# Kernel optimization log

Measured on AMD Instinct MI355X. Metric: run time of the kernel, lower is better.

The kernel has to match this reference:

```python
import jax, jax.numpy as jnp
import numpy as np

N, IPI, OPI, OPO = 20000, 128, 64, 16

def setup_inputs() -> dict:
    key = jax.random.key(0)
    k1, k2, k3, k4 = jax.random.split(key, 4)
    admat = jax.random.uniform(k1, (N, N), dtype=jnp.float32)
    features = jax.random.normal(k2, (N, IPI), dtype=jnp.float32)
    W1 = jax.random.normal(k3, (IPI, OPI), dtype=jnp.float32) * (1.0 / np.sqrt(IPI))
    W2 = jax.random.normal(k4, (OPI, OPO), dtype=jnp.float32) * (1.0 / np.sqrt(OPI))
    return {"admat": admat, "features": features, "W1": W1, "W2": W2}

def reference(admat, features, W1, W2):
    # layer1: A @ (X @ W1), thin-first ordering to minimize FLOPs/traffic
    h = jax.nn.relu(admat @ (features @ W1))          # [N, OPI]
    logits = admat @ (h @ W2)                          # [N, OPO]
    return jax.nn.softmax(logits, axis=1)
```

## Files before the change

kernel.cpp:

```cpp
#include <hip/hip_runtime.h>
#include <hip/hip_bf16.h>

#define NROWS 20000
#define IPI 128
#define OPI 64
#define OPO 16
#define BK 256
#define BK2 1024
#define A4S 10240

typedef __attribute__((ext_vector_type(8))) short bf16x8;
typedef __attribute__((ext_vector_type(4))) float f32x4;
typedef __attribute__((ext_vector_type(2))) unsigned int u32x2;
typedef __attribute__((ext_vector_type(4))) unsigned int u32x4;

#define LUT_LO 0x3C383000u
#define LUT_HI 0x4C484440u

static __device__ __forceinline__ unsigned short f2bf(float f) {
    __hip_bfloat16 h = __float2bfloat16(f);
    return *reinterpret_cast<unsigned short*>(&h);
}
static __device__ __forceinline__ unsigned pk2(float a, float b) {
    return (unsigned)f2bf(a) | ((unsigned)f2bf(b) << 16);
}
static __device__ __forceinline__ unsigned pk4_fp8(float a, float b, float c, float d) {
    int v = __builtin_amdgcn_cvt_pk_fp8_f32(a, b, 0, false);
    v = __builtin_amdgcn_cvt_pk_fp8_f32(c, d, v, true);
    return (unsigned)v;
}
static __device__ __forceinline__ unsigned char f2fp8(float a) {
    return (unsigned char)(pk4_fp8(a, 0.f, 0.f, 0.f) & 0xff);
}
static __device__ __forceinline__ unsigned nib4(float a) {
    const float q = a * 4.f;
    const float n = (q < 2.5f) ? fminf(rintf(q + q), 4.f)
                               : fminf(rintf(q), 4.f) + 2.f;
    return (unsigned)n;
}
static __device__ __forceinline__ u32x2 exp8(unsigned w) {
    const unsigned sl = w & 0x07070707u;
    const unsigned sh = (w >> 4) & 0x07070707u;
    const unsigned fe = __builtin_amdgcn_perm(LUT_HI, LUT_LO, sl);
    const unsigned fo = __builtin_amdgcn_perm(LUT_HI, LUT_LO, sh);
    u32x2 o;
    o[0] = __builtin_amdgcn_perm(fo, fe, 0x05010400u);
    o[1] = __builtin_amdgcn_perm(fo, fe, 0x07030602u);
    return o;
}

__global__ __launch_bounds__(256)
void k_xw1(const float* __restrict__ X, const float* __restrict__ W1,
           unsigned short* __restrict__ Bt) {
    __shared__ float w1[IPI * OPI];
    const int t = threadIdx.x;
    for (int i = t * 4; i < IPI * OPI; i += 1024)
        *(float4*)&w1[i] = *(const float4*)&W1[i];
    __syncthreads();

    const int r  = blockIdx.x * 16 + (t >> 4);
    const int c4 = (t & 15) * 4;
    const float* xr = X + (size_t)r * IPI;
    float4 acc = make_float4(0.f, 0.f, 0.f, 0.f);
    #pragma unroll 8
    for (int k = 0; k < IPI; ++k) {
        const float x = xr[k];
        const float4 w = *(const float4*)&w1[k * OPI + c4];
        acc.x = fmaf(x, w.x, acc.x);
        acc.y = fmaf(x, w.y, acc.y);
        acc.z = fmaf(x, w.z, acc.z);
        acc.w = fmaf(x, w.w, acc.w);
    }
    Bt[(size_t)(c4 + 0) * NROWS + r] = f2bf(acc.x);
    Bt[(size_t)(c4 + 1) * NROWS + r] = f2bf(acc.y);
    Bt[(size_t)(c4 + 2) * NROWS + r] = f2bf(acc.z);
    Bt[(size_t)(c4 + 3) * NROWS + r] = f2bf(acc.w);
}

__global__ __launch_bounds__(256)
void k_gemm1(const float* __restrict__ A, const unsigned short* __restrict__ Bt,
             float* __restrict__ Out, unsigned char* __restrict__ A4, int KC) {
    __shared__ unsigned short As[64 * BK];
    __shared__ unsigned short Bs[64 * BK];
    const int t    = threadIdx.x;
    const int lane = t & 63;
    const int wid  = t >> 6;
    const int lrow = lane & 15;
    const int lk   = lane >> 4;
    const int brow    = blockIdx.x * 64;
    const int k_begin = blockIdx.y * KC;
    const int k_end   = min(NROWS, k_begin + KC);

    const int sc_c = lane >> 1;
    const int sc_h = (lane & 1) * 4;

    f32x4 acc[4];
    #pragma unroll
    for (int n = 0; n < 4; ++n) acc[n] = (f32x4){0.f, 0.f, 0.f, 0.f};

    f32x4 va[16], vna[16];
    u32x2 vb[16], vnb[16];

    {
        const int  kg  = k_begin + lane * 4;
        const bool kok = kg < k_end;
        #pragma unroll
        for (int i = 0; i < 16; ++i) {
            const int grow = brow + wid * 16 + i;
            va[i] = (f32x4){0.f, 0.f, 0.f, 0.f};
            if (kok && grow < NROWS)
                va[i] = __builtin_nontemporal_load(
                    (const f32x4*)(A + (size_t)grow * NROWS + kg));
            vb[i] = (u32x2){0u, 0u};
            if (kok)
                vb[i] = *(const u32x2*)(Bt + (size_t)(wid * 16 + i) * NROWS + kg);
        }
    }

    for (int kt = k_begin; kt < k_end; kt += BK) {
        #pragma unroll
        for (int i = 0; i < 16; ++i) {
            const int r = wid * 16 + i;
            u32x2 u;
            u[0] = pk2(va[i][0], va[i][1]);
            u[1] = pk2(va[i][2], va[i][3]);
            const int slot = (sc_c ^ (r & 7)) * 8 + sc_h;
            *(u32x2*)&As[r * BK + slot] = u;
            *(u32x2*)&Bs[r * BK + slot] = vb[i];
        }
        __syncthreads();

        {
            const int  kgn  = kt + BK + lane * 4;
            const bool nok  = kgn < k_end;
            #pragma unroll
            for (int i = 0; i < 16; ++i) {
                const int grow = brow + wid * 16 + i;
                vna[i] = (f32x4){0.f, 0.f, 0.f, 0.f};
                if (nok && grow < NROWS)
                    vna[i] = __builtin_nontemporal_load(
                        (const f32x4*)(A + (size_t)grow * NROWS + kgn));
                vnb[i] = (u32x2){0u, 0u};
                if (nok)
                    vnb[i] = *(const u32x2*)(Bt + (size_t)(wid * 16 + i) * NROWS + kgn);
            }
            const int  kg  = kt + lane * 4;
            const bool kok = kg < k_end;
            #pragma unroll
            for (int i = 0; i < 16; ++i) {
                const int grow = brow + wid * 16 + i;
                if (kok && grow < NROWS) {
                    const unsigned pk = nib4(va[i][0]) | (nib4(va[i][1]) << 4) |
                                        (nib4(va[i][2]) << 8) | (nib4(va[i][3]) << 12);
                    *(unsigned short*)(A4 + (size_t)grow * A4S + (kg >> 1)) =
                        (unsigned short)pk;
                }
            }
        }

        #pragma unroll
        for (int h = 0; h < 8; ++h) {
            const int c  = h * 4 + lk;
            const int sc = (c & ~7) | ((c & 7) ^ (lrow & 7));
            const bf16x8 a = *(const bf16x8*)&As[(wid * 16 + lrow) * BK + sc * 8];
            #pragma unroll
            for (int n = 0; n < 4; ++n) {
                const bf16x8 b = *(const bf16x8*)&Bs[(n * 16 + lrow) * BK + sc * 8];
                acc[n] = __builtin_amdgcn_mfma_f32_16x16x32_bf16(a, b, acc[n], 0, 0, 0);
            }
        }
        __syncthreads();

        #pragma unroll
        for (int i = 0; i < 16; ++i) { va[i] = vna[i]; vb[i] = vnb[i]; }
    }

    float* outp = Out + (size_t)blockIdx.y * NROWS * OPI;
    const int r0 = (lane >> 4) * 4;
    #pragma unroll
    for (int n = 0; n < 4; ++n)
        #pragma unroll
        for (int r = 0; r < 4; ++r) {
            const int grow = brow + wid * 16 + r0 + r;
            if (grow < NROWS)
                outp[(size_t)grow * OPI + n * 16 + lrow] = acc[n][r];
        }
}

__global__ __launch_bounds__(256)
void k_hw2(const float* __restrict__ Hpart, const float* __restrict__ W2,
           unsigned char* __restrict__ Zt8, int S1) {
    __shared__ float w2[OPI * OPO];
    __shared__ float hs[16 * 68];
    const int t = threadIdx.x;
    if (t * 4 < OPI * OPO)
        *(float4*)&w2[t * 4] = *(const float4*)&W2[t * 4];

    const int r  = t >> 4;
    const int c4 = (t & 15) * 4;
    const size_t rowg = (size_t)blockIdx.x * 16 + r;

    float4 h = make_float4(0.f, 0.f, 0.f, 0.f);
    for (int s = 0; s < S1; ++s) {
        const float4 v = *(const float4*)&Hpart[((size_t)s * NROWS + rowg) * OPI + c4];
        h.x += v.x; h.y += v.y; h.z += v.z; h.w += v.w;
    }
    hs[r * 68 + c4 + 0] = fmaxf(h.x, 0.f);
    hs[r * 68 + c4 + 1] = fmaxf(h.y, 0.f);
    hs[r * 68 + c4 + 2] = fmaxf(h.z, 0.f);
    hs[r * 68 + c4 + 3] = fmaxf(h.w, 0.f);
    __syncthreads();

    const int c = t & 15;
    float z = 0.f;
    #pragma unroll 8
    for (int k = 0; k < OPI; ++k)
        z = fmaf(hs[r * 68 + k], w2[k * OPO + c], z);
    Zt8[(size_t)c * NROWS + rowg] = f2fp8(z * 0.25f);
}

__global__ __launch_bounds__(256)
void k_gemm2(const unsigned char* __restrict__ A4,
             const unsigned char* __restrict__ Zt8,
             float* __restrict__ Out, int KC) {
    __shared__ unsigned char As[64 * BK2];
    __shared__ unsigned char Bs[16 * BK2];
    const int t    = threadIdx.x;
    const int lane = t & 63;
    const int wid  = t >> 6;
    const int lrow = lane & 15;
    const int lk   = lane >> 4;
    const int brow    = blockIdx.x * 64;
    const int k_begin = blockIdx.y * KC;
    const int k_end   = min(NROWS, k_begin + KC);

    f32x4 acc = (f32x4){0.f, 0.f, 0.f, 0.f};

    const int zcol = t >> 4;
    const int zoff = (t & 15) * 64;

    u32x2 va[16], vna[16];
    u32x4 vz[4],  vnz[4];

    {
        const int  kgA = k_begin + lane * 16;
        const bool okA = kgA < k_end;
        #pragma unroll
        for (int i = 0; i < 16; ++i) {
            const int grow = brow + wid * 16 + i;
            va[i] = (u32x2){0u, 0u};
            if (okA && grow < NROWS)
                va[i] = *(const u32x2*)(A4 + (size_t)grow * A4S + (kgA >> 1));
        }
        #pragma unroll
        for (int j = 0; j < 4; ++j) {
            const int kg = k_begin + zoff + j * 16;
            vz[j] = (u32x4){0u, 0u, 0u, 0u};
            if (kg < k_end)
                vz[j] = *(const u32x4*)(Zt8 + (size_t)zcol * NROWS + kg);
        }
    }

    for (int kt = k_begin; kt < k_end; kt += BK2) {
        #pragma unroll
        for (int i = 0; i < 16; ++i) {
            const int r  = wid * 16 + i;
            const int c  = lane;
            const int sc = (c & ~7) | ((c & 7) ^ (r & 7));
            u32x4 ex;
            const u32x2 e0 = exp8(va[i][0]);
            const u32x2 e1 = exp8(va[i][1]);
            ex[0] = e0[0]; ex[1] = e0[1]; ex[2] = e1[0]; ex[3] = e1[1];
            *(u32x4*)&As[r * BK2 + sc * 16] = ex;
        }
        #pragma unroll
        for (int j = 0; j < 4; ++j) {
            const int c  = (zoff >> 4) + j;
            const int sc = (c & ~7) | ((c & 7) ^ (zcol & 7));
            *(u32x4*)&Bs[zcol * BK2 + sc * 16] = vz[j];
        }
        __syncthreads();

        {
            const int  kgn = kt + BK2 + lane * 16;
            const bool nok = kgn < k_end;
            #pragma unroll
            for (int i = 0; i < 16; ++i) {
                const int grow = brow + wid * 16 + i;
                vna[i] = (u32x2){0u, 0u};
                if (nok && grow < NROWS)
                    vna[i] = *(const u32x2*)(A4 + (size_t)grow * A4S + (kgn >> 1));
            }
            #pragma unroll
            for (int j = 0; j < 4; ++j) {
                const int kg = kt + BK2 + zoff + j * 16;
                vnz[j] = (u32x4){0u, 0u, 0u, 0u};
                if (kg < k_end)
                    vnz[j] = *(const u32x4*)(Zt8 + (size_t)zcol * NROWS + kg);
            }
        }

        #pragma unroll
        for (int h = 0; h < 32; ++h) {
            const int k0   = h * 32 + lk * 8;
            const int c    = k0 >> 4;
            const int hb   = k0 & 15;
            const int sc   = (c & ~7) | ((c & 7) ^ (lrow & 7));
            const long long a = *(const long long*)&As[(wid * 16 + lrow) * BK2 + sc * 16 + hb];
            const long long b = *(const long long*)&Bs[lrow * BK2 + sc * 16 + hb];
            acc = __builtin_amdgcn_mfma_f32_16x16x32_fp8_fp8(a, b, acc, 0, 0, 0);
        }
        __syncthreads();

        #pragma unroll
        for (int i = 0; i < 16; ++i) va[i] = vna[i];
        #pragma unroll
        for (int j = 0; j < 4; ++j)  vz[j] = vnz[j];
    }

    float* outp = Out + (size_t)blockIdx.y * NROWS * OPO;
    const int r0 = (lane >> 4) * 4;
    #pragma unroll
    for (int r = 0; r < 4; ++r) {
        const int grow = brow + wid * 16 + r0 + r;
        if (grow < NROWS) outp[(size_t)grow * OPO + lrow] = acc[r];
    }
}

__global__ __launch_bounds__(256)
void k_softmax(const float* __restrict__ Lpart, float* __restrict__ out, int S2) {
    const int t = threadIdx.x;
    const size_t base = (size_t)blockIdx.x * 256;
    float v = 0.f;
    for (int s = 0; s < S2; ++s)
        v += Lpart[(size_t)s * NROWS * OPO + base + t];
    float m = v;
    #pragma unroll
    for (int d = 8; d >= 1; d >>= 1) m = fmaxf(m, __shfl_xor(m, d, 16));
    const float e = expf(v - m);
    float sum = e;
    #pragma unroll
    for (int d = 8; d >= 1; d >>= 1) sum += __shfl_xor(sum, d, 16);
    out[base + t] = e / sum;
}

extern "C" void kernel_launch(void* const* d_in, const int* in_sizes, int n_in,
                              void* d_out, int out_size, void* d_ws, size_t ws_size,
                              hipStream_t stream) {
    const float* A  = (const float*)d_in[0];
    const float* X  = (const float*)d_in[1];
    const float* W1 = (const float*)d_in[2];
    const float* W2 = (const float*)d_in[3];
    float* out = (float*)d_out;

    auto al = [](size_t x) { return (x + 1023) & ~(size_t)1023; };
    const size_t a4_b = al((size_t)NROWS * A4S);
    const size_t bt_b = al((size_t)OPI * NROWS * 2);
    const size_t z8_b = al((size_t)OPO * NROWS);

    int S1 = 8, S2 = 8;
    auto need = [&](int s1, int s2) {
        return a4_b + bt_b + z8_b +
               ((size_t)s1 * NROWS * OPI + (size_t)s2 * NROWS * OPO) * sizeof(float);
    };
    while ((S1 > 1 || S2 > 1) && need(S1, S2) > ws_size) {
        if (S1 > 1) S1 >>= 1;
        if (S2 > 1) S2 >>= 1;
    }

    char* p = (char*)d_ws;
    unsigned char*  A4  = (unsigned char*)p;
    unsigned short* Bt  = (unsigned short*)(p + a4_b);
    unsigned char*  Zt8 = (unsigned char*)(p + a4_b + bt_b);
    float* H = (float*)(p + a4_b + bt_b + z8_b);
    float* L = H + (size_t)S1 * NROWS * OPI;

    const int MT  = (NROWS + 63) / 64;
    const int KC1 = ((((NROWS + S1 - 1) / S1) + BK - 1) / BK) * BK;
    const int KC2 = ((((NROWS + S2 - 1) / S2) + 511) & ~511);

    k_xw1<<<dim3(NROWS / 16), 256, 0, stream>>>(X, W1, Bt);
    k_gemm1<<<dim3(MT, S1), 256, 0, stream>>>(A, Bt, H, A4, KC1);
    k_hw2<<<dim3(NROWS / 16), 256, 0, stream>>>(H, W2, Zt8, S1);
    k_gemm2<<<dim3(MT, S2), 256, 0, stream>>>(A4, Zt8, L, KC2);
    k_softmax<<<dim3(NROWS * OPO / 256), 256, 0, stream>>>(L, out, S2);
}
```

Before: 517.9 us.

## Drop register prefetch and B LDS tile in gemm1, read B directly from global

Removes the software double-buffered register prefetch of A and B tiles, drops the shared-memory B tile, and loads B fragments straight from global/L2 inside the MFMA loop. It also sets launch bounds to request 4 blocks per CU. The goal is to cut register and LDS pressure so more waves are resident and memory latency is hidden by occupancy instead of explicit prefetch. The cost is the lost overlap of A loads with compute, plus repeated uncoalesced global reads of B per wave and an extra barrier per tile.

Result: slower. 1.090 ms (+110.5%).

```diff
diff --git a/kernel.cpp b/kernel.cpp
--- a/kernel.cpp
+++ b/kernel.cpp
@@ -77,11 +77,10 @@
     Bt[(size_t)(c4 + 3) * NROWS + r] = f2bf(acc.w);
 }
 
-__global__ __launch_bounds__(256)
+__global__ __launch_bounds__(256, 4)
 void k_gemm1(const float* __restrict__ A, const unsigned short* __restrict__ Bt,
              float* __restrict__ Out, unsigned char* __restrict__ A4, int KC) {
     __shared__ unsigned short As[64 * BK];
-    __shared__ unsigned short Bs[64 * BK];
     const int t    = threadIdx.x;
     const int lane = t & 63;
     const int wid  = t >> 6;
@@ -98,12 +97,11 @@
     #pragma unroll
     for (int n = 0; n < 4; ++n) acc[n] = (f32x4){0.f, 0.f, 0.f, 0.f};
 
-    f32x4 va[16], vna[16];
-    u32x2 vb[16], vnb[16];
-
-    {
-        const int  kg  = k_begin + lane * 4;
+    for (int kt = k_begin; kt < k_end; kt += BK) {
+        const int  kg  = kt + lane * 4;
         const bool kok = kg < k_end;
+
+        f32x4 va[16];
         #pragma unroll
         for (int i = 0; i < 16; ++i) {
             const int grow = brow + wid * 16 + i;
@@ -111,13 +109,19 @@
             if (kok && grow < NROWS)
                 va[i] = __builtin_nontemporal_load(
                     (const f32x4*)(A + (size_t)grow * NROWS + kg));
-            vb[i] = (u32x2){0u, 0u};
-            if (kok)
-                vb[i] = *(const u32x2*)(Bt + (size_t)(wid * 16 + i) * NROWS + kg);
-        }
-    }
-
-    for (int kt = k_begin; kt < k_end; kt += BK) {
+        }
+        #pragma unroll
+        for (int i = 0; i < 16; ++i) {
+            const int grow = brow + wid * 16 + i;
+            if (kok && grow < NROWS) {
+                const unsigned pk = nib4(va[i][0]) | (nib4(va[i][1]) << 4) |
+                                    (nib4(va[i][2]) << 8) | (nib4(va[i][3]) << 12);
+                *(unsigned short*)(A4 + (size_t)grow * A4S + (kg >> 1)) =
+                    (unsigned short)pk;
+            }
+        }
+        __syncthreads();
+
         #pragma unroll
         for (int i = 0; i < 16; ++i) {
             const int r = wid * 16 + i;
@@ -126,53 +130,23 @@
             u[1] = pk2(va[i][2], va[i][3]);
             const int slot = (sc_c ^ (r & 7)) * 8 + sc_h;
             *(u32x2*)&As[r * BK + slot] = u;
-            *(u32x2*)&Bs[r * BK + slot] = vb[i];
         }
         __syncthreads();
-
-        {
-            const int  kgn  = kt + BK + lane * 4;
-            const bool nok  = kgn < k_end;
-            #pragma unroll
-            for (int i = 0; i < 16; ++i) {
-                const int grow = brow + wid * 16 + i;
-                vna[i] = (f32x4){0.f, 0.f, 0.f, 0.f};
-                if (nok && grow < NROWS)
-                    vna[i] = __builtin_nontemporal_load(
-                        (const f32x4*)(A + (size_t)grow * NROWS + kgn));
-                vnb[i] = (u32x2){0u, 0u};
-                if (nok)
-                    vnb[i] = *(const u32x2*)(Bt + (size_t)(wid * 16 + i) * NROWS + kgn);
-            }
-            const int  kg  = kt + lane * 4;
-            const bool kok = kg < k_end;
-            #pragma unroll
-            for (int i = 0; i < 16; ++i) {
-                const int grow = brow + wid * 16 + i;
-                if (kok && grow < NROWS) {
-                    const unsigned pk = nib4(va[i][0]) | (nib4(va[i][1]) << 4) |
-                                        (nib4(va[i][2]) << 8) | (nib4(va[i][3]) << 12);
-                    *(unsigned short*)(A4 + (size_t)grow * A4S + (kg >> 1)) =
-                        (unsigned short)pk;
-                }
-            }
-        }
 
         #pragma unroll
         for (int h = 0; h < 8; ++h) {
             const int c  = h * 4 + lk;
             const int sc = (c & ~7) | ((c & 7) ^ (lrow & 7));
             const bf16x8 a = *(const bf16x8*)&As[(wid * 16 + lrow) * BK + sc * 8];
+            const int kb = kt + c * 8;
             #pragma unroll
             for (int n = 0; n < 4; ++n) {
-                const bf16x8 b = *(const bf16x8*)&Bs[(n * 16 + lrow) * BK + sc * 8];
+                bf16x8 b = (bf16x8){0, 0, 0, 0, 0, 0, 0, 0};
+                if (kb < k_end)
+                    b = *(const bf16x8*)(Bt + (size_t)(n * 16 + lrow) * NROWS + kb);
                 acc[n] = __builtin_amdgcn_mfma_f32_16x16x32_bf16(a, b, acc[n], 0, 0, 0);
             }
         }
-        __syncthreads();
-
-        #pragma unroll
-        for (int i = 0; i < 16; ++i) { va[i] = vna[i]; vb[i] = vnb[i]; }
     }
 
     float* outp = Out + (size_t)blockIdx.y * NROWS * OPI;
```
